# Performance work log

Measured on AMD Instinct MI355X. Metric: run time of the kernel, lower is better.

The kernel has to match this reference:

```python
import jax, jax.numpy as jnp
import numpy as np

B, S, V, E, P, C = 256, 128, 32000, 300, 200, 3
DIST_CUTOFF = 10

def _seq_mask(x):
    # TF: count_nonzero over seq, sequence_mask, expand to [B, S, 1]
    size = jnp.sum(x != 0, axis=1)
    m = (jnp.arange(S)[None, :] < size[:, None]).astype(jnp.float32)
    return m[:, :, None]

def _l2norm(w):
    n = jnp.sqrt(jnp.maximum(jnp.sum(w * w, axis=-1, keepdims=True), 1e-12))
    return w / n

def setup_inputs() -> dict:
    key = jax.random.key(0)
    ks = jax.random.split(key, 11)
    std = 0.01
    x1 = jax.random.randint(ks[0], (B, S), 0, V, dtype=jnp.int32)
    x2 = jax.random.randint(ks[1], (B, S), 0, V, dtype=jnp.int32)
    emb = jax.random.normal(ks[2], (V, E), jnp.float32)
    w_intra = jax.random.normal(ks[3], (E, E), jnp.float32) * std
    bias_intra = jax.random.normal(ks[4], (1,), jnp.float32) * std
    w_proj1 = jax.random.normal(ks[5], (2 * E, P), jnp.float32) * std
    w_proj2 = jax.random.normal(ks[6], (2 * E, P), jnp.float32) * std
    w_att = jax.random.normal(ks[7], (P, P), jnp.float32) * std
    w_cmp1 = jax.random.normal(ks[8], (2 * P, 2 * P), jnp.float32) * std
    w_cmp2 = jax.random.normal(ks[9], (2 * P, 2 * P), jnp.float32) * std
    w_agg = jax.random.normal(ks[10], (4 * P, C), jnp.float32) * std
    return dict(x1=x1, x2=x2, emb=emb, w_intra=w_intra, bias_intra=bias_intra,
                w_proj1=w_proj1, w_proj2=w_proj2, w_att=w_att,
                w_cmp1=w_cmp1, w_cmp2=w_cmp2, w_agg=w_agg)

def reference(x1, x2, emb, w_intra, bias_intra, w_proj1, w_proj2, w_att, w_cmp1, w_cmp2, w_agg):
    relu = jax.nn.relu
    mask1, mask2 = _seq_mask(x1), _seq_mask(x2)  # [B,S,1]

    # normalized embedding lookup
    e = _l2norm(emb)
    e1, e2 = e[x1], e[x2]  # [B,S,E]

    # intra-attention with distance bias (bias zeroed for |i-j| < 10)
    idx = jnp.arange(S)
    dist = jnp.abs(idx[None, :] - idx[:, None])
    dbias = bias_intra[0] * (dist >= DIST_CUTOFF).astype(jnp.float32)  # [S,S]

    def intra(x):
        f = relu(x @ w_intra)                       # shared F, [B,S,E]
        att = jnp.einsum('bik,bjk->bij', f, f)      # [B,S,S]
        sm = jax.nn.softmax(att + dbias[None], axis=2)
        xp = jnp.einsum('bik,bkj->bij', sm, x)
        return jnp.concatenate([x, xp], axis=2)     # [B,S,2E]

    e1, e2 = intra(e1), intra(e2)

    # project
    x1p = relu(e1 @ w_proj1)  # [B,S,P]
    x2p = relu(e2 @ w_proj2)

    # attend: F(x1) . F(x2), multiplicative mask, two softmaxes
    f1 = relu(x1p @ w_att)
    f2 = relu(x2p @ w_att)
    sim = jnp.einsum('bik,bjk->bij', f1, f2)          # [B,S1,S2]
    sim = sim * (mask1 * jnp.swapaxes(mask2, 1, 2))   # multiplicative mask (as in source)
    alpha = jnp.einsum('bki,bkj->bij', jax.nn.softmax(sim, axis=1), x1p)  # [B,S2,P]
    beta = jnp.einsum('bik,bkj->bij', jax.nn.softmax(sim, axis=2), x2p)   # [B,S1,P]

    # compare
    v1 = relu(jnp.concatenate([x1p, beta], axis=2) @ w_cmp1)
    v2 = relu(jnp.concatenate([x2p, alpha], axis=2) @ w_cmp2)

    # aggregate (masked sum pooling) + final ReLU projection (faithful to source)
    v1 = jnp.sum(v1 * mask1, axis=1)
    v2 = jnp.sum(v2 * mask2, axis=1)
    y_hat = relu(jnp.concatenate([v1, v2], axis=1) @ w_agg)  # [B,C]
    return y_hat
```

## Files before the change

### kernel.cpp

```cpp
#include <hip/hip_runtime.h>

#define BATCH 256
#define SEQ   128
#define EDIM  300
#define PDIM  200
#define BSTOK (BATCH * SEQ)

#define F_RELU  1
#define F_ACCUM 2

typedef unsigned short u16;
typedef __attribute__((ext_vector_type(8))) short bf16x8;
typedef __attribute__((ext_vector_type(4))) float f32x4;

__device__ __forceinline__ u16 f2bf(float x) {
    unsigned u = __float_as_uint(x);
    unsigned r = u + 0x7fffu + ((u >> 16) & 1u);
    return (u16)(r >> 16);
}
__device__ __forceinline__ float bf2f(u16 h) {
    return __uint_as_float(((unsigned)h) << 16);
}

__device__ __forceinline__ void split_store(const float* va, u16* dH, u16* dL)
// ... 51 lines not shown

__device__ __forceinline__ void gload_emb(float* va, const float* __restrict__ erow,
                                          int kb)
{
    if (kb + 16 <= EDIM) {
        #pragma unroll
        for (int i = 0; i < 4; i++) {
            const float4 v = *(const float4*)(erow + kb + i * 4);
            va[i * 4 + 0] = v.x; va[i * 4 + 1] = v.y;
            va[i * 4 + 2] = v.z; va[i * 4 + 3] = v.w;
        }
    } else {
        #pragma unroll
        for (int i = 0; i < 16; i++)
            va[i] = (kb + i < EDIM) ? erow[kb + i] : 0.f;
    }
}

__device__ __forceinline__ void commit_scale_split(float* va, float nrm,
                                                   u16* dH, u16* dL)
{
    #pragma unroll
    for (int i = 0; i < 16; i++) va[i] *= nrm;
    split_store(va, dH, dL);
}

__device__ __forceinline__ void commit_scale_hi(float* va, float nrm, u16* dH)
{
    #pragma unroll
    for (int i = 0; i < 16; i++) va[i] *= nrm;
    hi_store(va, dH);
}

#define MFMA3(ai, aj) \
    acc[ai][aj] = __builtin_amdgcn_mfma_f32_16x16x32_bf16(fah[ai], fbh[aj], acc[ai][aj], 0, 0, 0); \
    acc[ai][aj] = __builtin_amdgcn_mfma_f32_16x16x32_bf16(fah[ai], fbl[aj], acc[ai][aj], 0, 0, 0); \
    acc[ai][aj] = __builtin_amdgcn_mfma_f32_16x16x32_bf16(fal[ai], fbh[aj], acc[ai][aj], 0, 0, 0);

#define MFMA1(ai, aj) \
    acc[ai][aj] = __builtin_amdgcn_mfma_f32_16x16x32_bf16(fah[ai], fbh[aj], acc[ai][aj], 0, 0, 0);

__device__ __forceinline__ void store_transposed(
    float* __restrict__ PT, const f32x4 (*acc)[4], float* TR,
    int bn, int Nvalid, int wm, int wn, int lr, int quad, int tid, bool relu)
{
    #pragma unroll
    for (int h = 0; h < 2; h++) {
        __syncthreads();
        if ((wn >> 6) == h) {
            #pragma unroll
            for (int j = 0; j < 4; j++) {
                const int col = j * 16 + lr;
                #pragma unroll
                for (int i = 0; i < 4; i++)
                    #pragma unroll
                    for (int r = 0; r < 4; r++) {
                        float v = acc[i][j][r];
                        if (relu) v = fmaxf(v, 0.f);
                        TR[col * 129 + wm + i * 16 + quad * 4 + r] = v;
                    }
            }
        }
        __syncthreads();
        const int row = tid >> 2;
        const int gp = bn + h * 64 + row;
        if (gp < Nvalid) {
            float* dst = PT + (long long)gp * 128;
            for (int c = (tid & 3); c < 32; c += 4) {
                const int base = row * 129 + c * 4;
                *(float4*)(dst + c * 4) =
                    make_float4(TR[base], TR[base + 1], TR[base + 2], TR[base + 3]);
            }
        }
    }
}

__global__ __launch_bounds__(256) void gemm_proj(
    const int* __restrict__ x1, const int* __restrict__ x2,
    const float* __restrict__ emb, const float* __restrict__ norms,
    const u16* __restrict__ W1h, const u16* __restrict__ W1l,
    const u16* __restrict__ W2h, const u16* __restrict__ W2l,
    float* __restrict__ T, float* __restrict__ F0, float* __restrict__ F1)
{
    __shared__ __align__(16) unsigned char smem[40960];
    u16 (*AsH)[40] = (u16(*)[40])(smem);
    u16 (*AsL)[40] = (u16(*)[40])(smem + 10240);
    u16 (*BsH)[40] = (u16(*)[40])(smem + 20480);
    u16 (*BsL)[40] = (u16(*)[40])(smem + 30720);

    const int tid = threadIdx.x;
    const int id  = blockIdx.y * 5 + blockIdx.x;
    const int xcd = id & 7;
    const int s   = id >> 3;
    const int mt  = xcd + 8 * (s / 5);
    const int bm  = mt * 128;
    const int bn  = (s % 5) * 128;
    const bool side2 = mt >= 256;
    const bool wb = bn < 256;

    const u16* Bh = side2 ? W2h : W1h;
    const u16* Bl = side2 ? W2l : W1l;
    float* F = side2 ? F1 : F0;
    const int fm = side2 ? bm - 32768 : bm;
    const int* toks = (side2 ? x2 - 32768 : x1) + bm;

    const int wave = tid >> 6;
    const int lane = tid & 63;
    const int wm   = (wave >> 1) * 64;
    const int wn   = (wave & 1) * 64;
    const int lr   = lane & 15;
    const int quad = lane >> 4;
    const int sr   = tid >> 1;
    const int sc   = (tid & 1) * 16;

    const int tok = toks[sr];
    const float nrm = norms[tok];
    const float* erow = emb + (long long)tok * EDIM;

    const int gn = bn + sr;
    const bool bok = gn < 556;
    const u16* Bhp = Bh + (long long)gn * 320 + sc;
    const u16* Blp = Bl + (long long)gn * 320 + sc;

    f32x4 acc[4][4];
    #pragma unroll
    for (int i = 0; i < 4; i++)
        #pragma unroll
        for (int j = 0; j < 4; j++)
            acc[i][j] = (f32x4)(0.0f);

    float av[16];
    uint4 bh0, bh1, bl0, bl1;
    gload_emb(av, erow, sc);
    bh0 = bok ? *(const uint4*)(Bhp)     : make_uint4(0,0,0,0);
    bh1 = bok ? *(const uint4*)(Bhp + 8) : make_uint4(0,0,0,0);
    if (wb) {
        bl0 = bok ? *(const uint4*)(Blp)     : make_uint4(0,0,0,0);
        bl1 = bok ? *(const uint4*)(Blp + 8) : make_uint4(0,0,0,0);
    }

    for (int k0 = 0; k0 < 320; k0 += 32) {
        if (wb) commit_scale_split(av, nrm, &AsH[sr][sc], &AsL[sr][sc]);
        else    commit_scale_hi(av, nrm, &AsH[sr][sc]);
        *(uint4*)&BsH[sr][sc]     = bh0;
        *(uint4*)&BsH[sr][sc + 8] = bh1;
        if (wb) {
            *(uint4*)&BsL[sr][sc]     = bl0;
            *(uint4*)&BsL[sr][sc + 8] = bl1;
        }
        if (k0 + 32 < 320) {
            gload_emb(av, erow, k0 + 32 + sc);
            bh0 = bok ? *(const uint4*)(Bhp + k0 + 32)     : make_uint4(0,0,0,0);
            bh1 = bok ? *(const uint4*)(Bhp + k0 + 40)     : make_uint4(0,0,0,0);
            if (wb) {
                bl0 = bok ? *(const uint4*)(Blp + k0 + 32) : make_uint4(0,0,0,0);
                bl1 = bok ? *(const uint4*)(Blp + k0 + 40) : make_uint4(0,0,0,0);
            }
        }
        __syncthreads();

        bf16x8 fah[4], fal[4], fbh[4], fbl[4];
        #pragma unroll
        for (int i = 0; i < 4; i++) {
            fah[i] = *(const bf16x8*)&AsH[wm + i * 16 + lr][quad * 8];
            fbh[i] = *(const bf16x8*)&BsH[wn + i * 16 + lr][quad * 8];
        }
        if (wb) {
            #pragma unroll
            for (int i = 0; i < 4; i++) {
                fal[i] = *(const bf16x8*)&AsL[wm + i * 16 + lr][quad * 8];
                fbl[i] = *(const bf16x8*)&BsL[wn + i * 16 + lr][quad * 8];
            }
            #pragma unroll
            for (int i = 0; i < 4; i++)
                #pragma unroll
                for (int j = 0; j < 4; j++) { MFMA3(i, j) }
        } else {
            #pragma unroll
            for (int i = 0; i < 4; i++)
                #pragma unroll
                for (int j = 0; j < 4; j++) { MFMA1(i, j) }
        }
        __syncthreads();
    }

    if (wb) {
        float* Tb = T + (long long)mt * (PDIM * SEQ);
        store_transposed(Tb, acc, (float*)smem, bn, PDIM, wm, wn, lr, quad, tid, false);
    } else {
        #pragma unroll
        for (int i = 0; i < 4; i++) {
            #pragma unroll
            for (int j = 0; j < 4; j++) {
                const int idx = bn + wn + j * 16 + lr - 256;
                if (idx >= EDIM) continue;
                #pragma unroll
                for (int r = 0; r < 4; r++) {
                    const int gm = fm + wm + i * 16 + quad * 4 + r;
                    F[(long long)gm * EDIM + idx] = fmaxf(acc[i][j][r], 0.f);
                }
            }
        }
    }
}

__global__ __launch_bounds__(256) void gemm_xp(
    const float* __restrict__ P, float* __restrict__ T,
    const int* __restrict__ x1, const int* __restrict__ x2,
    const float* __restrict__ emb, const float* __restrict__ norms,
    const u16* __restrict__ W1h, const u16* __restrict__ W1l,
    const u16* __restrict__ W2h, const u16* __restrict__ W2l,
    float* __restrict__ XCAT)
{
    __shared__ __align__(16) unsigned char smem[40960];
    u16 (*AsH)[40] = (u16(*)[40])(smem);
    u16 (*AsL)[40] = (u16(*)[40])(smem + 10240);
    u16 (*BsH)[40] = (u16(*)[40])(smem + 20480);
    u16 (*BsL)[40] = (u16(*)[40])(smem + 30720);

    const int tid = threadIdx.x;
    const int bz  = blockIdx.z;
    const int bn  = blockIdx.x * 128;

    const int wave = tid >> 6;
    const int lane = tid & 63;
    const int wm   = (wave >> 1) * 64;
    const int wn   = (wave & 1) * 64;
    const int lr   = lane & 15;
    const int quad = lane >> 4;
    const int sr   = tid >> 1;
    const int sc   = (tid & 1) * 16;

    const int* toks = (bz < BATCH) ? x1 + bz * SEQ : x2 + (bz - BATCH) * SEQ;
    const u16* Wh = (bz < BATCH) ? W1h : W2h;
    const u16* Wl = (bz < BATCH) ? W1l : W2l;
    const int tok = toks[sr];
    const float nrm = norms[tok];
    const float* erow = emb + (long long)tok * EDIM;
    const float* Pb = P + (long long)bz * (SEQ * SEQ);
    float* Tb = T + (long long)bz * (PDIM * SEQ);

    const int gn = bn + sr;
    const bool bok = gn < PDIM;
    const u16* Whp = Wh + (long long)gn * 320 + sc;
    const u16* Wlp = Wl + (long long)gn * 320 + sc;
    const float* Pp = Pb + (long long)sr * 128 + sc;
    const float* Tp = Tb + (long long)gn * 128 + sc;

    f32x4 acc[4][4];
    #pragma unroll
    for (int i = 0; i < 4; i++)
        #pragma unroll
        for (int j = 0; j < 4; j++)
            acc[i][j] = (f32x4)(0.0f);

    float av[16], bv[16];
    uint4 bh0, bh1, bl0, bl1;
    gload_emb(av, erow, sc);
    bh0 = bok ? *(const uint4*)(Whp)     : make_uint4(0,0,0,0);
    bh1 = bok ? *(const uint4*)(Whp + 8) : make_uint4(0,0,0,0);
    bl0 = bok ? *(const uint4*)(Wlp)     : make_uint4(0,0,0,0);
    bl1 = bok ? *(const uint4*)(Wlp + 8) : make_uint4(0,0,0,0);

    for (int k0 = 0; k0 < 320; k0 += 32) {
        commit_scale_split(av, nrm, &AsH[sr][sc], &AsL[sr][sc]);
        *(uint4*)&BsH[sr][sc]     = bh0;
        *(uint4*)&BsH[sr][sc + 8] = bh1;
        *(uint4*)&BsL[sr][sc]     = bl0;
        *(uint4*)&BsL[sr][sc + 8] = bl1;
        if (k0 + 32 < 320) {
            gload_emb(av, erow, k0 + 32 + sc);
            bh0 = bok ? *(const uint4*)(Whp + k0 + 32) : make_uint4(0,0,0,0);
            bh1 = bok ? *(const uint4*)(Whp + k0 + 40) : make_uint4(0,0,0,0);
            bl0 = bok ? *(const uint4*)(Wlp + k0 + 32) : make_uint4(0,0,0,0);
            bl1 = bok ? *(const uint4*)(Wlp + k0 + 40) : make_uint4(0,0,0,0);
        } else {
            gload16(av, Pp, true);
            gload16(bv, Tp, bok);
        }
        __syncthreads();

        bf16x8 fah[4], fal[4], fbh[4], fbl[4];
        #pragma unroll
        for (int i = 0; i < 4; i++) {
            fah[i] = *(const bf16x8*)&AsH[wm + i * 16 + lr][quad * 8];
            fal[i] = *(const bf16x8*)&AsL[wm + i * 16 + lr][quad * 8];
            fbh[i] = *(const bf16x8*)&BsH[wn + i * 16 + lr][quad * 8];
            fbl[i] = *(const bf16x8*)&BsL[wn + i * 16 + lr][quad * 8];
        }
        #pragma unroll
        for (int i = 0; i < 4; i++)
            #pragma unroll
            for (int j = 0; j < 4; j++) { MFMA3(i, j) }
        __syncthreads();
    }

    for (int k0 = 0; k0 < 128; k0 += 32) {
        split_store(av, &AsH[sr][sc], &AsL[sr][sc]);
        split_store(bv, &BsH[sr][sc], &BsL[sr][sc]);
        if (k0 + 32 < 128) {
            gload16(av, Pp + k0 + 32, true);
            gload16(bv, Tp + k0 + 32, bok);
        }
        __syncthreads();

        bf16x8 fah[4], fal[4], fbh[4], fbl[4];
        #pragma unroll
        for (int i = 0; i < 4; i++) {
            fah[i] = *(const bf16x8*)&AsH[wm + i * 16 + lr][quad * 8];
            fal[i] = *(const bf16x8*)&AsL[wm + i * 16 + lr][quad * 8];
            fbh[i] = *(const bf16x8*)&BsH[wn + i * 16 + lr][quad * 8];
            fbl[i] = *(const bf16x8*)&BsL[wn + i * 16 + lr][quad * 8];
        }
        #pragma unroll
        for (int i = 0; i < 4; i++)
            #pragma unroll
            for (int j = 0; j < 4; j++) { MFMA3(i, j) }
        __syncthreads();
    }

    const long long rowbase = (long long)bz * SEQ;
    #pragma unroll
    for (int i = 0; i < 4; i++) {
        #pragma unroll
        for (int j = 0; j < 4; j++) {
            const int gnn = bn + wn + j * 16 + lr;
            if (gnn >= PDIM) continue;
            #pragma unroll
            for (int r = 0; r < 4; r++) {
                const int gm = wm + i * 16 + quad * 4 + r;
                XCAT[(rowbase + gm) * 400 + gnn] = fmaxf(acc[i][j][r], 0.f);
            }
        }
    }
    store_transposed(Tb, acc, (float*)smem, bn, PDIM, wm, wn, lr, quad, tid, true);
}

template <int NM>
__global__ __launch_bounds__(256) void gemm_flat(
    const float* __restrict__ A,
    const u16* __restrict__ Bh, const u16* __restrict__ Bl,
    const u16* __restrict__ Bh2, const u16* __restrict__ Bl2, int Msplit,
    float* __restrict__ C, float* __restrict__ PO, const int* __restrict__ sizes,
    int M, int N, int Kp, int lda, int ldb, int ldc, int flags)
{
    __shared__ u16 AsH[128][40];
    __shared__ u16 AsL[128][40];
    __shared__ u16 BsH[128][40];
    __shared__ u16 BsL[128][40];

    const int tid = threadIdx.x;
    int bx = blockIdx.x, by = blockIdx.y;
    if ((gridDim.y & 7) == 0) {
        const int gx = gridDim.x;
        const int id = by * gx + bx;
        const int xcd = id & 7;
        const int s = id >> 3;
        by = xcd + 8 * (s / gx);
        bx = s % gx;
    }
    const int bm = by * 128;
    const int bn = bx * 128;

    const int wave = tid >> 6;
    const int lane = tid & 63;
    const int wm   = (wave >> 1) * 64;
    const int wn   = (wave & 1) * 64;
    const int lr   = lane & 15;
    const int quad = lane >> 4;
    const int sr   = tid >> 1;
    const int sc   = (tid & 1) * 16;

    if (bm >= Msplit) { Bh = Bh2; Bl = Bl2; }

    const float* Ap = A + (long long)(bm + sr) * lda + sc;
    const int gn = bn + sr;
    const bool bok = gn < N;
    const u16* Bhp = Bh + (long long)gn * ldb + sc;
    const u16* Blp = Bl + (long long)gn * ldb + sc;

    f32x4 acc[4][4];
    #pragma unroll
    for (int i = 0; i < 4; i++)
        #pragma unroll
        for (int j = 0; j < 4; j++)
            acc[i][j] = (f32x4)(0.0f);

    float av[16];
    uint4 bh0, bh1, bl0, bl1;
    gload16(av, Ap, true);
    bh0 = bok ? *(const uint4*)(Bhp)     : make_uint4(0,0,0,0);
    bh1 = bok ? *(const uint4*)(Bhp + 8) : make_uint4(0,0,0,0);
    if constexpr (NM == 3) {
        bl0 = bok ? *(const uint4*)(Blp)     : make_uint4(0,0,0,0);
        bl1 = bok ? *(const uint4*)(Blp + 8) : make_uint4(0,0,0,0);
    }

    for (int k0 = 0; k0 < Kp; k0 += 32) {
        if constexpr (NM == 3) split_store(av, &AsH[sr][sc], &AsL[sr][sc]);
        else                   hi_store(av, &AsH[sr][sc]);
        *(uint4*)&BsH[sr][sc]     = bh0;
        *(uint4*)&BsH[sr][sc + 8] = bh1;
        if constexpr (NM == 3) {
            *(uint4*)&BsL[sr][sc]     = bl0;
            *(uint4*)&BsL[sr][sc + 8] = bl1;
        }
        if (k0 + 32 < Kp) {
            gload16(av, Ap + k0 + 32, true);
            bh0 = bok ? *(const uint4*)(Bhp + k0 + 32) : make_uint4(0,0,0,0);
            bh1 = bok ? *(const uint4*)(Bhp + k0 + 40) : make_uint4(0,0,0,0);
            if constexpr (NM == 3) {
                bl0 = bok ? *(const uint4*)(Blp + k0 + 32) : make_uint4(0,0,0,0);
                bl1 = bok ? *(const uint4*)(Blp + k0 + 40) : make_uint4(0,0,0,0);
            }
        }
        __syncthreads();

        bf16x8 fah[4], fal[4], fbh[4], fbl[4];
        #pragma unroll
        for (int i = 0; i < 4; i++) {
            fah[i] = *(const bf16x8*)&AsH[wm + i * 16 + lr][quad * 8];
            fbh[i] = *(const bf16x8*)&BsH[wn + i * 16 + lr][quad * 8];
        }
        if constexpr (NM == 3) {
            #pragma unroll
            for (int i = 0; i < 4; i++) {
                fal[i] = *(const bf16x8*)&AsL[wm + i * 16 + lr][quad * 8];
                fbl[i] = *(const bf16x8*)&BsL[wn + i * 16 + lr][quad * 8];
            }
            #pragma unroll
            for (int i = 0; i < 4; i++)
                #pragma unroll
                for (int j = 0; j < 4; j++) { MFMA3(i, j) }
        } else {
            #pragma unroll
            for (int i = 0; i < 4; i++)
                #pragma unroll
                for (int j = 0; j < 4; j++) { MFMA1(i, j) }
        }
        __syncthreads();
    }

    const int sz = PO ? sizes[bm >> 7] : 0;
    float ps[4] = {0.f, 0.f, 0.f, 0.f};
    #pragma unroll
    for (int j = 0; j < 4; j++) {
        const int gnn = bn + wn + j * 16 + lr;
        const bool gok = gnn < N;
        #pragma unroll
        for (int i = 0; i < 4; i++) {
            #pragma unroll
            for (int r = 0; r < 4; r++) {
                const int row = wm + i * 16 + quad * 4 + r;
                const int gm = bm + row;
                float v = acc[i][j][r];
                if (flags & F_RELU) v = fmaxf(v, 0.f);
                if (gok && C) C[(long long)gm * ldc + gnn] = v;
                if (PO && row < sz) ps[j] += v;
            }
        }
    }
    if (PO) {
        #pragma unroll
        for (int j = 0; j < 4; j++) {
            ps[j] += __shfl_xor(ps[j], 16);
            ps[j] += __shfl_xor(ps[j], 32);
        }
        float* PS = (float*)AsH;
        if (wm == 0 && quad == 0) {
            #pragma unroll
            for (int j = 0; j < 4; j++) PS[wn + j * 16 + lr] = ps[j];
        }
        __syncthreads();
        if (wm == 64 && quad == 0) {
            #pragma unroll
            for (int j = 0; j < 4; j++) PS[wn + j * 16 + lr] += ps[j];
        }
        __syncthreads();
        if (tid < 128) {
            const int gnn = bn + tid;
            if (gnn < N) PO[(long long)(bm >> 7) * N + gnn] = PS[tid];
        }
    }
}

template <int MODE>
__global__ __launch_bounds__(256) void gemm_bat(
    const float* __restrict__ A, const float* __restrict__ Aalt,
    const float* __restrict__ B, const float* __restrict__ Balt,
    float* __restrict__ C, float* __restrict__ PT,
    int N, int Kvalid, int Kp, int lda, int ldb, int ldc,
    long long sA, long long sB, long long sC, long long sPT,
    int flags, const float* __restrict__ bias_ptr, const int* __restrict__ sizes,
    int same_ab)
{
    constexpr int NM = (MODE == 0) ? 3 : 1;
    constexpr int SB = (MODE >= 1) ? 65536 : 40960;
    __shared__ __align__(16) unsigned char smem[SB];
    u16 (*AsH)[40] = (u16(*)[40])(smem);
    u16 (*AsL)[40] = (u16(*)[40])(smem + 10240);
    u16 (*BsH)[40] = (u16(*)[40])(smem + 20480);
    u16 (*BsL)[40] = (u16(*)[40])(smem + 30720);

    const int bz = blockIdx.z;
    long long zb = bz;
    const float* Ause = A;
    const float* Buse = B;
    if (Aalt && bz >= BATCH) { Ause = Aalt; Buse = Balt; zb = bz - BATCH; }
    Ause += zb * sA;
    Buse += zb * sB;
    C += (long long)bz * sC;
    if (PT) PT += (long long)bz * sPT;

    const int tid  = threadIdx.x;
    const int bn   = blockIdx.x * 128;
    const int wave = tid >> 6;
    const int lane = tid & 63;
    const int wm   = (wave >> 1) * 64;
    const int wn   = (wave & 1) * 64;
    const int lr   = lane & 15;
    const int quad = lane >> 4;
    const int sr   = tid >> 1;
    const int sc   = (tid & 1) * 16;

    f32x4 acc[4][4];
    #pragma unroll
    for (int i = 0; i < 4; i++)
        #pragma unroll
        for (int j = 0; j < 4; j++)
            acc[i][j] = (f32x4)(0.0f);

    u16 (*fbH)[40] = same_ab ? AsH : BsH;
    u16 (*fbL)[40] = same_ab ? AsL : BsL;

    const float* Apt = Ause + (long long)sr * lda + sc;
    const int gn = bn + sr;
    const bool bok = gn < N;
    const float* Bpt = Buse + (long long)gn * ldb + sc;

    float av[16], bv[16];
    gload16(av, Apt, true);
    if (!same_ab) gload16(bv, Bpt, bok);

    for (int k0 = 0; k0 < Kp; k0 += 32) {
        kmask16(av, k0 + sc, Kvalid);
        if constexpr (NM == 3) split_store(av, &AsH[sr][sc], &AsL[sr][sc]);
        else                   hi_store(av, &AsH[sr][sc]);
        if (!same_ab) {
            kmask16(bv, k0 + sc, Kvalid);
            if constexpr (NM == 3) split_store(bv, &BsH[sr][sc], &BsL[sr][sc]);
            else                   hi_store(bv, &BsH[sr][sc]);
        }
        if (k0 + 32 < Kp) {
            gload16(av, Apt + k0 + 32, true);
            if (!same_ab) gload16(bv, Bpt + k0 + 32, bok);
        }
        __syncthreads();

        bf16x8 fah[4], fal[4], fbh[4], fbl[4];
        #pragma unroll
        for (int i = 0; i < 4; i++) {
            fah[i] = *(const bf16x8*)&AsH[wm + i * 16 + lr][quad * 8];
            fbh[i] = *(const bf16x8*)&fbH[wn + i * 16 + lr][quad * 8];
        }
        if constexpr (NM == 3) {
            #pragma unroll
            for (int i = 0; i < 4; i++) {
                fal[i] = *(const bf16x8*)&AsL[wm + i * 16 + lr][quad * 8];
                fbl[i] = *(const bf16x8*)&fbL[wn + i * 16 + lr][quad * 8];
            }
            #pragma unroll
            for (int i = 0; i < 4; i++)
                #pragma unroll
                for (int j = 0; j < 4; j++) { MFMA3(i, j) }
        } else {
            #pragma unroll
            for (int i = 0; i < 4; i++)
                #pragma unroll
                for (int j = 0; j < 4; j++) { MFMA1(i, j) }
        }
        __syncthreads();
    }

    if (MODE == 1) {
        float* S = (float*)smem;
        const float bias = bias_ptr[0];
        #pragma unroll
        for (int i = 0; i < 4; i++) {
            #pragma unroll
            for (int j = 0; j < 4; j++) {
                const int col = wn + j * 16 + lr;
                #pragma unroll
                for (int r = 0; r < 4; r++) {
                    const int row = wm + i * 16 + quad * 4 + r;
                    int d = row - col; d = d < 0 ? -d : d;
                    S[row * 128 + col] = acc[i][j][r] + ((d >= 10) ? bias : 0.f);
                }
            }
        }
        __syncthreads();
        const int row = tid >> 1;
        const int half = (tid & 1) * 64;
        float mx = -1e30f;
        for (int c = 0; c < 64; c++) mx = fmaxf(mx, S[row * 128 + half + c]);
        mx = fmaxf(mx, __shfl_xor(mx, 1));
        float sum = 0.f;
        for (int c = 0; c < 64; c++) sum += __expf(S[row * 128 + half + c] - mx);
        sum += __shfl_xor(sum, 1);
        const float inv = 1.f / sum;
        for (int c = 0; c < 64; c++)
            C[(long long)row * ldc + half + c] = __expf(S[row * 128 + half + c] - mx) * inv;
    } else if (MODE == 2) {
        float* S = (float*)smem;
        const int s1 = sizes[bz];
        const int s2 = sizes[BATCH + bz];
        #pragma unroll
        for (int i = 0; i < 4; i++) {
            #pragma unroll
            for (int j = 0; j < 4; j++) {
                const int col = wn + j * 16 + lr;
                #pragma unroll
                for (int r = 0; r < 4; r++) {
                    const int row = wm + i * 16 + quad * 4 + r;
                    float v = acc[i][j][r];
                    if (row >= s1 || col >= s2) v = 0.f;
                    S[row * 128 + col] = v;
                }
            }
        }
        __syncthreads();
        const int idx = tid >> 1;
        const int half = (tid & 1) * 64;
        {
            float mx = -1e30f;
            for (int c = 0; c < 64; c++) mx = fmaxf(mx, S[idx * 128 + half + c]);
            mx = fmaxf(mx, __shfl_xor(mx, 1));
            float sum = 0.f;
            for (int c = 0; c < 64; c++) sum += __expf(S[idx * 128 + half + c] - mx);
            sum += __shfl_xor(sum, 1);
            const float inv = 1.f / sum;
            for (int c = 0; c < 64; c++)
                C[(long long)idx * 128 + half + c] = __expf(S[idx * 128 + half + c] - mx) * inv;
        }
        {
            float mx = -1e30f;
            for (int r = 0; r < 64; r++) mx = fmaxf(mx, S[(half + r) * 128 + idx]);
            mx = fmaxf(mx, __shfl_xor(mx, 1));
            float sum = 0.f;
            for (int r = 0; r < 64; r++) sum += __expf(S[(half + r) * 128 + idx] - mx);
            sum += __shfl_xor(sum, 1);
            const float inv = 1.f / sum;
            for (int r = 0; r < 64; r++)
                PT[(long long)idx * 128 + half + r] = __expf(S[(half + r) * 128 + idx] - mx) * inv;
        }
    } else {
        const int s1 = sizes ? sizes[bz] : SEQ;
        const int s2 = sizes ? sizes[BATCH + bz] : SEQ;
        #pragma unroll
        for (int i = 0; i < 4; i++) {
            #pragma unroll
            for (int j = 0; j < 4; j++) {
                const int gnn = bn + wn + j * 16 + lr;
                if (gnn >= N) continue;
                #pragma unroll
                for (int r = 0; r < 4; r++) {
                    const int gm = wm + i * 16 + quad * 4 + r;
                    float v = acc[i][j][r];
                    if (sizes && (gm >= s1 || gnn >= s2)) v = 0.f;
                    if (flags & F_ACCUM) v += C[(long long)gm * ldc + gnn];
                    if (flags & F_RELU)  v = fmaxf(v, 0.f);
                    C[(long long)gm * ldc + gnn] = v;
                    if (PT) PT[(long long)gnn * 128 + gm] = v;
                }
            }
        }
    }
}

struct WEnt { const float* src; u16* H; u16* L; int K, N, Kp, rowStart; };
struct WTab { WEnt e[11]; };
__global__ void convert_all(WTab t)
{
    const int row = blockIdx.y;
    const int k = blockIdx.x * 256 + threadIdx.x;
    #pragma unroll
    for (int s = 0; s < 11; s++) {
        const WEnt w = t.e[s];
        if (row >= w.rowStart && row < w.rowStart + w.N) {
            const int n = row - w.rowStart;
            if (k < w.Kp) {
                const float v = (k < w.K) ? w.src[(long long)k * w.N + n] : 0.f;
                const u16 h = f2bf(v);
                w.H[(long long)n * w.Kp + k] = h;
                w.L[(long long)n * w.Kp + k] = f2bf(v - bf2f(h));
            }
            return;
        }
    }
}

__global__ void norms_kernel(const float* __restrict__ emb, float* __restrict__ norms)
{
    const int r = blockIdx.x;
    const int lane = threadIdx.x;
    const float* row = emb + (long long)r * EDIM;
    float ss = 0.f;
    #pragma unroll
    for (int i = 0; i < 5; i++) {
        const int c = lane + i * 64;
        const float f = (c < EDIM) ? row[c] : 0.f;
        ss += f * f;
    }
    #pragma unroll
    for (int o = 32; o > 0; o >>= 1) ss += __shfl_xor(ss, o);
    if (lane == 0) norms[r] = rsqrtf(fmaxf(ss, 1e-12f));
}

__global__ void sizes_kernel(const int* __restrict__ x1, const int* __restrict__ x2,
                             int* __restrict__ sizes)
{
    const int b = blockIdx.x;
    const int side = blockIdx.y;
    const int* x = (side ? x2 : x1) + b * SEQ;
    const int nz = (x[threadIdx.x] != 0) ? 1 : 0;
    const unsigned long long bal = __ballot(nz);
    __shared__ int part[2];
    if ((threadIdx.x & 63) == 0) part[threadIdx.x >> 6] = __popcll(bal);
    __syncthreads();
    if (threadIdx.x == 0) sizes[side * BATCH + b] = part[0] + part[1];
}

__global__ void agg_kernel(const float* __restrict__ v1s, const float* __restrict__ v2s,
                           const float* __restrict__ w_agg, float* __restrict__ y)
{
    const int b = blockIdx.x;
    const int lane = threadIdx.x;
// ... 123 lines not shown
```

Measured before the change: 557.2 us.

## Double-buffer LDS tiles in all GEMMs and vectorize softmax epilogues

Converts the projection, xp, flat and batched GEMM main loops to ping-pong LDS buffers, so the next tile is committed to shared memory while MFMAs consume the current one. This removes one barrier per k-step and overlaps global loads with compute. The xp kernel's two K loops are merged into a single 14-stage pipeline. Softmax epilogues now use a padded row stride (132) and float4 shared-memory and global accesses. The cost is doubled LDS per block (up to 80KB), which may reduce occupancy.

```diff
diff --git a/kernel.cpp b/kernel.cpp
--- a/kernel.cpp
+++ b/kernel.cpp
@@ -157,11 +157,7 @@
     const u16* __restrict__ W2h, const u16* __restrict__ W2l,
     float* __restrict__ T, float* __restrict__ F0, float* __restrict__ F1)
 {
-    __shared__ __align__(16) unsigned char smem[40960];
-    u16 (*AsH)[40] = (u16(*)[40])(smem);
-    u16 (*AsL)[40] = (u16(*)[40])(smem + 10240);
-    u16 (*BsH)[40] = (u16(*)[40])(smem + 20480);
-    u16 (*BsL)[40] = (u16(*)[40])(smem + 30720);
+    __shared__ __align__(16) unsigned char smem[81920];
 
     const int tid = threadIdx.x;
     const int id  = blockIdx.y * 5 + blockIdx.x;
@@ -206,51 +202,68 @@
 
     float av[16];
     uint4 bh0, bh1, bl0, bl1;
-    gload_emb(av, erow, sc);
-    bh0 = bok ? *(const uint4*)(Bhp)     : make_uint4(0,0,0,0);
-    bh1 = bok ? *(const uint4*)(Bhp + 8) : make_uint4(0,0,0,0);
-    if (wb) {
-        bl0 = bok ? *(const uint4*)(Blp)     : make_uint4(0,0,0,0);
-        bl1 = bok ? *(const uint4*)(Blp + 8) : make_uint4(0,0,0,0);
-    }
-
-    for (int k0 = 0; k0 < 320; k0 += 32) {
-        if (wb) commit_scale_split(av, nrm, &AsH[sr][sc], &AsL[sr][sc]);
-        else    commit_scale_hi(av, nrm, &AsH[sr][sc]);
-        *(uint4*)&BsH[sr][sc]     = bh0;
-        *(uint4*)&BsH[sr][sc + 8] = bh1;
+
+#define PROJ_LOAD(sidx) do { \
+    const int kk_ = (sidx) * 32; \
+    gload_emb(av, erow, kk_ + sc); \
+    bh0 = bok ? *(const uint4*)(Bhp + kk_)     : make_uint4(0,0,0,0); \
+    bh1 = bok ? *(const uint4*)(Bhp + kk_ + 8) : make_uint4(0,0,0,0); \
+    if (wb) { \
+        bl0 = bok ? *(const uint4*)(Blp + kk_)     : make_uint4(0,0,0,0); \
+        bl1 = bok ? *(const uint4*)(Blp + kk_ + 8) : make_uint4(0,0,0,0); \
+    } \
+} while (0)
+
+#define PROJ_COMMIT(bufp) do { \
+    u16 (*cAsH)[40] = (u16(*)[40])(bufp); \
+    u16 (*cAsL)[40] = (u16(*)[40])((bufp) + 10240); \
+    u16 (*cBsH)[40] = (u16(*)[40])((bufp) + 20480); \
+    u16 (*cBsL)[40] = (u16(*)[40])((bufp) + 30720); \
+    if (wb) commit_scale_split(av, nrm, &cAsH[sr][sc], &cAsL[sr][sc]); \
+    else    commit_scale_hi(av, nrm, &cAsH[sr][sc]); \
+    *(uint4*)&cBsH[sr][sc]     = bh0; \
+    *(uint4*)&cBsH[sr][sc + 8] = bh1; \
+    if (wb) { \
+        *(uint4*)&cBsL[sr][sc]     = bl0; \
+        *(uint4*)&cBsL[sr][sc + 8] = bl1; \
+    } \
+} while (0)
+
+    PROJ_LOAD(0);
+    PROJ_COMMIT(smem);
+    PROJ_LOAD(1);
+    __syncthreads();
+
+    for (int t = 0; t < 10; ++t) {
+        unsigned char* rb  = smem + (t & 1) * 40960;
+        unsigned char* wbb = smem + ((t & 1) ^ 1) * 40960;
+        u16 (*rAsH)[40] = (u16(*)[40])(rb);
+        u16 (*rAsL)[40] = (u16(*)[40])(rb + 10240);
+        u16 (*rBsH)[40] = (u16(*)[40])(rb + 20480);
+        u16 (*rBsL)[40] = (u16(*)[40])(rb + 30720);
+
+        bf16x8 fah[4], fbh[4];
+        #pragma unroll
+        for (int i = 0; i < 4; i++) {
+            fah[i] = *(const bf16x8*)&rAsH[wm + i * 16 + lr][quad * 8];
+            fbh[i] = *(const bf16x8*)&rBsH[wn + i * 16 + lr][quad * 8];
+        }
         if (wb) {
-            *(uint4*)&BsL[sr][sc]     = bl0;
-            *(uint4*)&BsL[sr][sc + 8] = bl1;
-        }
-        if (k0 + 32 < 320) {
-            gload_emb(av, erow, k0 + 32 + sc);
-            bh0 = bok ? *(const uint4*)(Bhp + k0 + 32)     : make_uint4(0,0,0,0);
-            bh1 = bok ? *(const uint4*)(Bhp + k0 + 40)     : make_uint4(0,0,0,0);
-            if (wb) {
-                bl0 = bok ? *(const uint4*)(Blp + k0 + 32) : make_uint4(0,0,0,0);
-                bl1 = bok ? *(const uint4*)(Blp + k0 + 40) : make_uint4(0,0,0,0);
-            }
-        }
-        __syncthreads();
-
-        bf16x8 fah[4], fal[4], fbh[4], fbl[4];
-        #pragma unroll
-        for (int i = 0; i < 4; i++) {
-            fah[i] = *(const bf16x8*)&AsH[wm + i * 16 + lr][quad * 8];
-            fbh[i] = *(const bf16x8*)&BsH[wn + i * 16 + lr][quad * 8];
-        }
-        if (wb) {
+            bf16x8 fal[4], fbl[4];
             #pragma unroll
             for (int i = 0; i < 4; i++) {
-                fal[i] = *(const bf16x8*)&AsL[wm + i * 16 + lr][quad * 8];
-                fbl[i] = *(const bf16x8*)&BsL[wn + i * 16 + lr][quad * 8];
-            }
+                fal[i] = *(const bf16x8*)&rAsL[wm + i * 16 + lr][quad * 8];
+                fbl[i] = *(const bf16x8*)&rBsL[wn + i * 16 + lr][quad * 8];
+            }
+            if (t < 9) PROJ_COMMIT(wbb);
+            if (t < 8) PROJ_LOAD(t + 2);
             #pragma unroll
             for (int i = 0; i < 4; i++)
                 #pragma unroll
                 for (int j = 0; j < 4; j++) { MFMA3(i, j) }
         } else {
+            if (t < 9) PROJ_COMMIT(wbb);
+            if (t < 8) PROJ_LOAD(t + 2);
             #pragma unroll
             for (int i = 0; i < 4; i++)
                 #pragma unroll
@@ -258,6 +271,8 @@
         }
         __syncthreads();
     }
+#undef PROJ_LOAD
+#undef PROJ_COMMIT
 
     if (wb) {
         float* Tb = T + (long long)mt * (PDIM * SEQ);
@@ -287,11 +302,7 @@
     const u16* __restrict__ W2h, const u16* __restrict__ W2l,
     float* __restrict__ XCAT)
 {
-    __shared__ __align__(16) unsigned char smem[40960];
-    u16 (*AsH)[40] = (u16(*)[40])(smem);
-    u16 (*AsL)[40] = (u16(*)[40])(smem + 10240);
-    u16 (*BsH)[40] = (u16(*)[40])(smem + 20480);
-    u16 (*BsL)[40] = (u16(*)[40])(smem + 30720);
+    __shared__ __align__(16) unsigned char smem[81920];
 
     const int tid = threadIdx.x;
     const int bz  = blockIdx.z;
@@ -331,68 +342,70 @@
 
     float av[16], bv[16];
     uint4 bh0, bh1, bl0, bl1;
-    gload_emb(av, erow, sc);
-    bh0 = bok ? *(const uint4*)(Whp)     : make_uint4(0,0,0,0);
-    bh1 = bok ? *(const uint4*)(Whp + 8) : make_uint4(0,0,0,0);
-    bl0 = bok ? *(const uint4*)(Wlp)     : make_uint4(0,0,0,0);
-    bl1 = bok ? *(const uint4*)(Wlp + 8) : make_uint4(0,0,0,0);
-
-    for (int k0 = 0; k0 < 320; k0 += 32) {
-        commit_scale_split(av, nrm, &AsH[sr][sc], &AsL[sr][sc]);
-        *(uint4*)&BsH[sr][sc]     = bh0;
-        *(uint4*)&BsH[sr][sc + 8] = bh1;
-        *(uint4*)&BsL[sr][sc]     = bl0;
-        *(uint4*)&BsL[sr][sc + 8] = bl1;
-        if (k0 + 32 < 320) {
-            gload_emb(av, erow, k0 + 32 + sc);
-            bh0 = bok ? *(const uint4*)(Whp + k0 + 32) : make_uint4(0,0,0,0);
-            bh1 = bok ? *(const uint4*)(Whp + k0 + 40) : make_uint4(0,0,0,0);
-            bl0 = bok ? *(const uint4*)(Wlp + k0 + 32) : make_uint4(0,0,0,0);
-            bl1 = bok ? *(const uint4*)(Wlp + k0 + 40) : make_uint4(0,0,0,0);
-        } else {
-            gload16(av, Pp, true);
-            gload16(bv, Tp, bok);
-        }
-        __syncthreads();
+
+#define XP_LOAD(sidx) do { \
+    if ((sidx) < 10) { \
+        const int kk_ = (sidx) * 32; \
+        gload_emb(av, erow, kk_ + sc); \
+        bh0 = bok ? *(const uint4*)(Whp + kk_)     : make_uint4(0,0,0,0); \
+        bh1 = bok ? *(const uint4*)(Whp + kk_ + 8) : make_uint4(0,0,0,0); \
+        bl0 = bok ? *(const uint4*)(Wlp + kk_)     : make_uint4(0,0,0,0); \
+        bl1 = bok ? *(const uint4*)(Wlp + kk_ + 8) : make_uint4(0,0,0,0); \
+    } else { \
+        const int kk_ = ((sidx) - 10) * 32; \
+        gload16(av, Pp + kk_, true); \
+        gload16(bv, Tp + kk_, bok); \
+    } \
+} while (0)
+
+#define XP_COMMIT(sidx, bufp) do { \
+    u16 (*cAsH)[40] = (u16(*)[40])(bufp); \
+    u16 (*cAsL)[40] = (u16(*)[40])((bufp) + 10240); \
+    u16 (*cBsH)[40] = (u16(*)[40])((bufp) + 20480); \
+    u16 (*cBsL)[40] = (u16(*)[40])((bufp) + 30720); \
+    if ((sidx) < 10) { \
+        commit_scale_split(av, nrm, &cAsH[sr][sc], &cAsL[sr][sc]); \
+        *(uint4*)&cBsH[sr][sc]     = bh0; \
+        *(uint4*)&cBsH[sr][sc + 8] = bh1; \
+        *(uint4*)&cBsL[sr][sc]     = bl0; \
+        *(uint4*)&cBsL[sr][sc + 8] = bl1; \
+    } else { \
+        split_store(av, &cAsH[sr][sc], &cAsL[sr][sc]); \
+        split_store(bv, &cBsH[sr][sc], &cBsL[sr][sc]); \
+    } \
+} while (0)
+
+    XP_LOAD(0);
+    XP_COMMIT(0, smem);
+    XP_LOAD(1);
+    __syncthreads();
+
+    for (int t = 0; t < 14; ++t) {
+        unsigned char* rb  = smem + (t & 1) * 40960;
+        unsigned char* wbb = smem + ((t & 1) ^ 1) * 40960;
+        u16 (*rAsH)[40] = (u16(*)[40])(rb);
+        u16 (*rAsL)[40] = (u16(*)[40])(rb + 10240);
+        u16 (*rBsH)[40] = (u16(*)[40])(rb + 20480);
+        u16 (*rBsL)[40] = (u16(*)[40])(rb + 30720);
 
         bf16x8 fah[4], fal[4], fbh[4], fbl[4];
         #pragma unroll
         for (int i = 0; i < 4; i++) {
-            fah[i] = *(const bf16x8*)&AsH[wm + i * 16 + lr][quad * 8];
-            fal[i] = *(const bf16x8*)&AsL[wm + i * 16 + lr][quad * 8];
-            fbh[i] = *(const bf16x8*)&BsH[wn + i * 16 + lr][quad * 8];
-            fbl[i] = *(const bf16x8*)&BsL[wn + i * 16 + lr][quad * 8];
-        }
+            fah[i] = *(const bf16x8*)&rAsH[wm + i * 16 + lr][quad * 8];
+            fal[i] = *(const bf16x8*)&rAsL[wm + i * 16 + lr][quad * 8];
+            fbh[i] = *(const bf16x8*)&rBsH[wn + i * 16 + lr][quad * 8];
+            fbl[i] = *(const bf16x8*)&rBsL[wn + i * 16 + lr][quad * 8];
+        }
+        if (t < 13) XP_COMMIT(t + 1, wbb);
+        if (t < 12) XP_LOAD(t + 2);
         #pragma unroll
         for (int i = 0; i < 4; i++)
             #pragma unroll
             for (int j = 0; j < 4; j++) { MFMA3(i, j) }
         __syncthreads();
     }
-
-    for (int k0 = 0; k0 < 128; k0 += 32) {
-        split_store(av, &AsH[sr][sc], &AsL[sr][sc]);
-        split_store(bv, &BsH[sr][sc], &BsL[sr][sc]);
-        if (k0 + 32 < 128) {
-            gload16(av, Pp + k0 + 32, true);
-            gload16(bv, Tp + k0 + 32, bok);
-        }
-        __syncthreads();
-
-        bf16x8 fah[4], fal[4], fbh[4], fbl[4];
-        #pragma unroll
-        for (int i = 0; i < 4; i++) {
-            fah[i] = *(const bf16x8*)&AsH[wm + i * 16 + lr][quad * 8];
-            fal[i] = *(const bf16x8*)&AsL[wm + i * 16 + lr][quad * 8];
-            fbh[i] = *(const bf16x8*)&BsH[wn + i * 16 + lr][quad * 8];
-            fbl[i] = *(const bf16x8*)&BsL[wn + i * 16 + lr][quad * 8];
-        }
-        #pragma unroll
-        for (int i = 0; i < 4; i++)
-            #pragma unroll
-            for (int j = 0; j < 4; j++) { MFMA3(i, j) }
-        __syncthreads();
-    }
+#undef XP_LOAD
+#undef XP_COMMIT
 
     const long long rowbase = (long long)bz * SEQ;
     #pragma unroll
@@ -419,10 +432,9 @@
     float* __restrict__ C, float* __restrict__ PO, const int* __restrict__ sizes,
     int M, int N, int Kp, int lda, int ldb, int ldc, int flags)
 {
-    __shared__ u16 AsH[128][40];
-    __shared__ u16 AsL[128][40];
-    __shared__ u16 BsH[128][40];
-    __shared__ u16 BsL[128][40];
+    constexpr int BUFB = (NM == 3) ? 40960 : 20480;
+    constexpr int BOFF = (NM == 3) ? 20480 : 10240;
+    __shared__ __align__(16) unsigned char smem[2 * BUFB];
 
     const int tid = threadIdx.x;
     int bx = blockIdx.x, by = blockIdx.y;
@@ -463,51 +475,70 @@
 
     float av[16];
     uint4 bh0, bh1, bl0, bl1;
-    gload16(av, Ap, true);
-    bh0 = bok ? *(const uint4*)(Bhp)     : make_uint4(0,0,0,0);
-    bh1 = bok ? *(const uint4*)(Bhp + 8) : make_uint4(0,0,0,0);
-    if constexpr (NM == 3) {
-        bl0 = bok ? *(const uint4*)(Blp)     : make_uint4(0,0,0,0);
-        bl1 = bok ? *(const uint4*)(Blp + 8) : make_uint4(0,0,0,0);
-    }
-
-    for (int k0 = 0; k0 < Kp; k0 += 32) {
-        if constexpr (NM == 3) split_store(av, &AsH[sr][sc], &AsL[sr][sc]);
-        else                   hi_store(av, &AsH[sr][sc]);
-        *(uint4*)&BsH[sr][sc]     = bh0;
-        *(uint4*)&BsH[sr][sc + 8] = bh1;
+
+#define FLAT_LOAD(sidx) do { \
+    const int kk_ = (sidx) * 32; \
+    gload16(av, Ap + kk_, true); \
+    bh0 = bok ? *(const uint4*)(Bhp + kk_)     : make_uint4(0,0,0,0); \
+    bh1 = bok ? *(const uint4*)(Bhp + kk_ + 8) : make_uint4(0,0,0,0); \
+    if constexpr (NM == 3) { \
+        bl0 = bok ? *(const uint4*)(Blp + kk_)     : make_uint4(0,0,0,0); \
+        bl1 = bok ? *(const uint4*)(Blp + kk_ + 8) : make_uint4(0,0,0,0); \
+    } \
+} while (0)
+
+#define FLAT_COMMIT(bufp) do { \
+    u16 (*cAsH)[40] = (u16(*)[40])(bufp); \
+    u16 (*cBsH)[40] = (u16(*)[40])((bufp) + BOFF); \
+    if constexpr (NM == 3) { \
+        u16 (*cAsL)[40] = (u16(*)[40])((bufp) + 10240); \
+        u16 (*cBsL)[40] = (u16(*)[40])((bufp) + 30720); \
+        split_store(av, &cAsH[sr][sc], &cAsL[sr][sc]); \
+        *(uint4*)&cBsL[sr][sc]     = bl0; \
+        *(uint4*)&cBsL[sr][sc + 8] = bl1; \
+    } else { \
+        hi_store(av, &cAsH[sr][sc]); \
+    } \
+    *(uint4*)&cBsH[sr][sc]     = bh0; \
+    *(uint4*)&cBsH[sr][sc + 8] = bh1; \
+} while (0)
+
+    const int NT = Kp >> 5;
+    FLAT_LOAD(0);
+    FLAT_COMMIT(smem);
+    FLAT_LOAD(1);
+    __syncthreads();
+
+    for (int t = 0; t < NT; ++t) {
+        unsigned char* rb  = smem + (t & 1) * BUFB;
+        unsigned char* wbb = smem + ((t & 1) ^ 1) * BUFB;
+        u16 (*rAsH)[40] = (u16(*)[40])(rb);
+        u16 (*rBsH)[40] = (u16(*)[40])(rb + BOFF);
+
+        bf16x8 fah[4], fbh[4];
+        #pragma unroll
+        for (int i = 0; i < 4; i++) {
+            fah[i] = *(const bf16x8*)&rAsH[wm + i * 16 + lr][quad * 8];
+            fbh[i] = *(const bf16x8*)&rBsH[wn + i * 16 + lr][quad * 8];
+        }
         if constexpr (NM == 3) {
-            *(uint4*)&BsL[sr][sc]     = bl0;
-            *(uint4*)&BsL[sr][sc + 8] = bl1;
-        }
-        if (k0 + 32 < Kp) {
-            gload16(av, Ap + k0 + 32, true);
-            bh0 = bok ? *(const uint4*)(Bhp + k0 + 32) : make_uint4(0,0,0,0);
-            bh1 = bok ? *(const uint4*)(Bhp + k0 + 40) : make_uint4(0,0,0,0);
-            if constexpr (NM == 3) {
-                bl0 = bok ? *(const uint4*)(Blp + k0 + 32) : make_uint4(0,0,0,0);
-                bl1 = bok ? *(const uint4*)(Blp + k0 + 40) : make_uint4(0,0,0,0);
-            }
-        }
-        __syncthreads();
-
-        bf16x8 fah[4], fal[4], fbh[4], fbl[4];
-        #pragma unroll
-        for (int i = 0; i < 4; i++) {
-            fah[i] = *(const bf16x8*)&AsH[wm + i * 16 + lr][quad * 8];
-            fbh[i] = *(const bf16x8*)&BsH[wn + i * 16 + lr][quad * 8];
-        }
-        if constexpr (NM == 3) {
+            u16 (*rAsL)[40] = (u16(*)[40])(rb + 10240);
+            u16 (*rBsL)[40] = (u16(*)[40])(rb + 30720);
+            bf16x8 fal[4], fbl[4];
             #pragma unroll
             for (int i = 0; i < 4; i++) {
-                fal[i] = *(const bf16x8*)&AsL[wm + i * 16 + lr][quad * 8];
-                fbl[i] = *(const bf16x8*)&BsL[wn + i * 16 + lr][quad * 8];
-            }
+                fal[i] = *(const bf16x8*)&rAsL[wm + i * 16 + lr][quad * 8];
+                fbl[i] = *(const bf16x8*)&rBsL[wn + i * 16 + lr][quad * 8];
+            }
+            if (t < NT - 1) FLAT_COMMIT(wbb);
+            if (t < NT - 2) FLAT_LOAD(t + 2);
             #pragma unroll
             for (int i = 0; i < 4; i++)
                 #pragma unroll
                 for (int j = 0; j < 4; j++) { MFMA3(i, j) }
         } else {
+            if (t < NT - 1) FLAT_COMMIT(wbb);
+            if (t < NT - 2) FLAT_LOAD(t + 2);
             #pragma unroll
             for (int i = 0; i < 4; i++)
                 #pragma unroll
@@ -515,6 +546,8 @@
         }
         __syncthreads();
     }
+#undef FLAT_LOAD
+#undef FLAT_COMMIT
 
     const int sz = PO ? sizes[bm >> 7] : 0;
     float ps[4] = {0.f, 0.f, 0.f, 0.f};
@@ -541,7 +574,7 @@
             ps[j] += __shfl_xor(ps[j], 16);
             ps[j] += __shfl_xor(ps[j], 32);
         }
-        float* PS = (float*)AsH;
+        float* PS = (float*)smem;
         if (wm == 0 && quad == 0) {
             #pragma unroll
             for (int j = 0; j < 4; j++) PS[wn + j * 16 + lr] = ps[j];
@@ -559,6 +592,7 @@
     }
 }
 
+#define SLD 132
 template <int MODE>
 __global__ __launch_bounds__(256) void gemm_bat(
     const float* __restrict__ A, const float* __restrict__ Aalt,
@@ -570,12 +604,10 @@
     int same_ab)
 {
     constexpr int NM = (MODE == 0) ? 3 : 1;
-    constexpr int SB = (MODE >= 1) ? 65536 : 40960;
-    __shared__ __align__(16) unsigned char smem[SB];
-    u16 (*AsH)[40] = (u16(*)[40])(smem);
-    u16 (*AsL)[40] = (u16(*)[40])(smem + 10240);
-    u16 (*BsH)[40] = (u16(*)[40])(smem + 20480);
-    u16 (*BsL)[40] = (u16(*)[40])(smem + 30720);
+    constexpr int BUFB = (NM == 3) ? 40960 : 20480;
+    constexpr int BOFF = (NM == 3) ? 20480 : 10240;
+    constexpr int SMB  = (MODE == 0) ? 2 * 40960 : (128 * SLD * 4);
+    __shared__ __align__(16) unsigned char smem[SMB];
 
     const int bz = blockIdx.z;
     long long zb = bz;
@@ -605,50 +637,77 @@
         for (int j = 0; j < 4; j++)
             acc[i][j] = (f32x4)(0.0f);
 
-    u16 (*fbH)[40] = same_ab ? AsH : BsH;
-    u16 (*fbL)[40] = same_ab ? AsL : BsL;
-
     const float* Apt = Ause + (long long)sr * lda + sc;
     const int gn = bn + sr;
     const bool bok = gn < N;
     const float* Bpt = Buse + (long long)gn * ldb + sc;
 
     float av[16], bv[16];
-    gload16(av, Apt, true);
-    if (!same_ab) gload16(bv, Bpt, bok);
-
-    for (int k0 = 0; k0 < Kp; k0 += 32) {
-        kmask16(av, k0 + sc, Kvalid);
-        if constexpr (NM == 3) split_store(av, &AsH[sr][sc], &AsL[sr][sc]);
-        else                   hi_store(av, &AsH[sr][sc]);
-        if (!same_ab) {
-            kmask16(bv, k0 + sc, Kvalid);
-            if constexpr (NM == 3) split_store(bv, &BsH[sr][sc], &BsL[sr][sc]);
-            else                   hi_store(bv, &BsH[sr][sc]);
-        }
-        if (k0 + 32 < Kp) {
-            gload16(av, Apt + k0 + 32, true);
-            if (!same_ab) gload16(bv, Bpt + k0 + 32, bok);
-        }
-        __syncthreads();
-
-        bf16x8 fah[4], fal[4], fbh[4], fbl[4];
+
+#define BAT_LOAD(sidx) do { \
+    const int kk_ = (sidx) * 32; \
+    gload16(av, Apt + kk_, true); \
+    if (!same_ab) gload16(bv, Bpt + kk_, bok); \
+} while (0)
+
+#define BAT_COMMIT(sidx, bufp) do { \
+    u16 (*cAsH)[40] = (u16(*)[40])(bufp); \
+    u16 (*cBsH)[40] = (u16(*)[40])((bufp) + BOFF); \
+    kmask16(av, (sidx) * 32 + sc, Kvalid); \
+    if constexpr (NM == 3) { \
+        u16 (*cAsL)[40] = (u16(*)[40])((bufp) + 10240); \
+        split_store(av, &cAsH[sr][sc], &cAsL[sr][sc]); \
+    } else { \
+        hi_store(av, &cAsH[sr][sc]); \
+    } \
+    if (!same_ab) { \
+        kmask16(bv, (sidx) * 32 + sc, Kvalid); \
+        if constexpr (NM == 3) { \
+            u16 (*cBsL)[40] = (u16(*)[40])((bufp) + 30720); \
+            split_store(bv, &cBsH[sr][sc], &cBsL[sr][sc]); \
+        } else { \
+            hi_store(bv, &cBsH[sr][sc]); \
+        } \
+    } \
+} while (0)
+
+    const int NT = Kp >> 5;
+    BAT_LOAD(0);
+    BAT_COMMIT(0, smem);
+    BAT_LOAD(1);
+    __syncthreads();
+
+    for (int t = 0; t < NT; ++t) {
+        unsigned char* rb  = smem + (t & 1) * BUFB;
+        unsigned char* wbb = smem + ((t & 1) ^ 1) * BUFB;
+        u16 (*rAsH)[40] = (u16(*)[40])(rb);
+        u16 (*rBsH)[40] = same_ab ? (u16(*)[40])(rb) : (u16(*)[40])(rb + BOFF);
+
+        bf16x8 fah[4], fbh[4];
         #pragma unroll
         for (int i = 0; i < 4; i++) {
-            fah[i] = *(const bf16x8*)&AsH[wm + i * 16 + lr][quad * 8];
-            fbh[i] = *(const bf16x8*)&fbH[wn + i * 16 + lr][quad * 8];
+            fah[i] = *(const bf16x8*)&rAsH[wm + i * 16 + lr][quad * 8];
+            fbh[i] = *(const bf16x8*)&rBsH[wn + i * 16 + lr][quad * 8];
         }
         if constexpr (NM == 3) {
+            u16 (*rAsL)[40] = (u16(*)[40])(rb + 10240);
+            u16 (*rBsL)[40] = same_ab ? (u16(*)[40])(rb + 10240)
+                                      : (u16(*)[40])(rb + 30720);
+            bf16x8 fal[4], fbl[4];
             #pragma unroll
             for (int i = 0; i < 4; i++) {
-                fal[i] = *(const bf16x8*)&AsL[wm + i * 16 + lr][quad * 8];
-                fbl[i] = *(const bf16x8*)&fbL[wn + i * 16 + lr][quad * 8];
-            }
+                fal[i] = *(const bf16x8*)&rAsL[wm + i * 16 + lr][quad * 8];
+                fbl[i] = *(const bf16x8*)&rBsL[wn + i * 16 + lr][quad * 8];
+            }
+            if (t < NT - 1) BAT_COMMIT(t + 1, wbb);
+            if (t < NT - 2) BAT_LOAD(t + 2);
             #pragma unroll
             for (int i = 0; i < 4; i++)
                 #pragma unroll
                 for (int j = 0; j < 4; j++) { MFMA3(i, j) }
         } else {
+            if (t < NT - 1) BAT_COMMIT(t + 1, wbb);
+            if (t < NT - 2) BAT_LOAD(t + 2);
             #pragma unroll
             for (int i = 0; i < 4; i++)
                 #pragma unroll
@@ -656,6 +715,8 @@
         }
         __syncthreads();
     }
+#undef BAT_LOAD
+#undef BAT_COMMIT
 
     if (MODE == 1) {
         float* S = (float*)smem;
@@ -669,22 +730,38 @@
                 for (int r = 0; r < 4; r++) {
                     const int row = wm + i * 16 + quad * 4 + r;
                     int d = row - col; d = d < 0 ? -d : d;
-                    S[row * 128 + col] = acc[i][j][r] + ((d >= 10) ? bias : 0.f);
+                    S[row * SLD + col] = acc[i][j][r] + ((d >= 10) ? bias : 0.f);
                 }
             }
         }
         __syncthreads();
         const int row = tid >> 1;
         const int half = (tid & 1) * 64;
+        float* Sr = S + row * SLD + half;
         float mx = -1e30f;
-        for (int c = 0; c < 64; c++) mx = fmaxf(mx, S[row * 128 + half + c]);
+        #pragma unroll
+        for (int c = 0; c < 16; c++) {
+            const float4 v = *(const float4*)(Sr + c * 4);
+            mx = fmaxf(fmaxf(fmaxf(mx, v.x), fmaxf(v.y, v.z)), v.w);
+        }
         mx = fmaxf(mx, __shfl_xor(mx, 1));
         float sum = 0.f;
-        for (int c = 0; c < 64; c++) sum += __expf(S[row * 128 + half + c] - mx);
+        #pragma unroll
+        for (int c = 0; c < 16; c++) {
+            float4 v = *(const float4*)(Sr + c * 4);
+            v.x = __expf(v.x - mx); v.y = __expf(v.y - mx);
+            v.z = __expf(v.z - mx); v.w = __expf(v.w - mx);
+            sum += (v.x + v.y) + (v.z + v.w);
+            *(float4*)(Sr + c * 4) = v;
+        }
         sum += __shfl_xor(sum, 1);
         const float inv = 1.f / sum;
-        for (int c = 0; c < 64; c++)
-            C[(long long)row * ldc + half + c] = __expf(S[row * 128 + half + c] - mx) * inv;
+        #pragma unroll
+        for (int c = 0; c < 16; c++) {
+            float4 v = *(const float4*)(Sr + c * 4);
+            v.x *= inv; v.y *= inv; v.z *= inv; v.w *= inv;
+            *(float4*)&C[(long long)row * ldc + half + c * 4] = v;
+        }
     } else if (MODE == 2) {
         float* S = (float*)smem;
         const int s1 = sizes[bz];
@@ -699,7 +776,7 @@
                     const int row = wm + i * 16 + quad * 4 + r;
                     float v = acc[i][j][r];
                     if (row >= s1 || col >= s2) v = 0.f;
-                    S[row * 128 + col] = v;
+                    S[row * SLD + col] = v;
                 }
             }
         }
@@ -707,26 +784,51 @@
         const int idx = tid >> 1;
         const int half = (tid & 1) * 64;
         {
+            const float* Sr = S + idx * SLD + half;
             float mx = -1e30f;
-            for (int c = 0; c < 64; c++) mx = fmaxf(mx, S[idx * 128 + half + c]);
+            #pragma unroll
+            for (int c = 0; c < 16; c++) {
+                const float4 v = *(const float4*)(Sr + c * 4);
+                mx = fmaxf(fmaxf(fmaxf(mx, v.x), fmaxf(v.y, v.z)), v.w);
+            }
             mx = fmaxf(mx, __shfl_xor(mx, 1));
             float sum = 0.f;
-            for (int c = 0; c < 64; c++) sum += __expf(S[idx * 128 + half + c] - mx);
+            #pragma unroll
+            for (int c = 0; c < 16; c++) {
+                const float4 v = *(const float4*)(Sr + c * 4);
+                sum += (__expf(v.x - mx) + __expf(v.y - mx))
+                     + (__expf(v.z - mx) + __expf(v.w - mx));
+            }
             sum += __shfl_xor(sum, 1);
             const float inv = 1.f / sum;
-            for (int c = 0; c < 64; c++)
-                C[(long long)idx * 128 + half + c] = __expf(S[idx * 128 + half + c] - mx) * inv;
+            #pragma unroll
+            for (int c = 0; c < 16; c++) {
+                const float4 v = *(const float4*)(Sr + c * 4);
+                float4 o;
+                o.x = __expf(v.x - mx) * inv; o.y = __expf(v.y - mx) * inv;
+                o.z = __expf(v.z - mx) * inv; o.w = __expf(v.w - mx) * inv;
+                *(float4*)&C[(long long)idx * 128 + half + c * 4] = o;
+            }
         }
         {
             float mx = -1e30f;
-            for (int r = 0; r < 64; r++) mx = fmaxf(mx, S[(half + r) * 128 + idx]);
+            for (int r = 0; r < 64; r++)
+                mx = fmaxf(mx, S[(half + r) * SLD + idx]);
             mx = fmaxf(mx, __shfl_xor(mx, 1));
             float sum = 0.f;
-            for (int r = 0; r < 64; r++) sum += __expf(S[(half + r) * 128 + idx] - mx);
+            for (int r = 0; r < 64; r++)
+                sum += __expf(S[(half + r) * SLD + idx] - mx);
             sum += __shfl_xor(sum, 1);
             const float inv = 1.f / sum;
-            for (int r = 0; r < 64; r++)
-                PT[(long long)idx * 128 + half + r] = __expf(S[(half + r) * 128 + idx] - mx) * inv;
+            #pragma unroll
+            for (int r4 = 0; r4 < 16; r4++) {
+                float4 o;
+                o.x = __expf(S[(half + r4 * 4 + 0) * SLD + idx] - mx) * inv;
+                o.y = __expf(S[(half + r4 * 4 + 1) * SLD + idx] - mx) * inv;
+                o.z = __expf(S[(half + r4 * 4 + 2) * SLD + idx] - mx) * inv;
+                o.w = __expf(S[(half + r4 * 4 + 3) * SLD + idx] - mx) * inv;
+                *(float4*)&PT[(long long)idx * 128 + half + r4 * 4] = o;
+            }
         }
     } else {
         const int s1 = sizes ? sizes[bz] : SEQ;
```

New measurement: 575.0 us. 3.2% more time.
